# Kernel optimization log

Measured on AMD Instinct MI355X. Metric: run time of the kernel, lower is better.

Reference implementation:

```python
import jax, jax.numpy as jnp
import numpy as np

EMB = 128
BINS = 32
CUT = 5.0
NLAYER = 5
NHID = 4  # extra hidden linears in edge MLP (hidden_dim_list has 5 entries total)
N_NODES = 50000
N_EDGES = 800000
N_GRAPH = 256
NODE_CLASS = 100


def setup_inputs() -> dict:
    key = jax.random.key(0)
    ks = jax.random.split(key, 20)
    s = 0.02
    inp = {
        'z': jax.random.randint(ks[0], (N_NODES,), 0, NODE_CLASS),
        'pos': jax.random.normal(ks[1], (N_NODES, 3), dtype=jnp.float32) * 3.0,
        'batch': jnp.sort(jax.random.randint(ks[2], (N_NODES,), 0, N_GRAPH)),
        'edge_index': jax.random.randint(ks[3], (2, N_EDGES), 0, N_NODES),
        # parameters
        'atom_table': jax.random.normal(ks[4], (NODE_CLASS, EMB), dtype=jnp.float32) * s,
        'atom_w': jax.random.normal(ks[5], (EMB, EMB), dtype=jnp.float32) * s,
        'atom_b': jnp.zeros((EMB,), jnp.float32),
        'edge_emb_w': jax.random.normal(ks[6], (BINS, EMB), dtype=jnp.float32) * s,
        'edge_emb_b': jnp.zeros((EMB,), jnp.float32),
        'edge_w0': jax.random.normal(ks[7], (NLAYER, 3 * EMB, EMB), dtype=jnp.float32) * s,
        'edge_b0': jnp.zeros((NLAYER, EMB), jnp.float32),
        'edge_w': jax.random.normal(ks[8], (NLAYER, NHID, EMB, EMB), dtype=jnp.float32) * s,
        'edge_b': jnp.zeros((NLAYER, NHID, EMB), jnp.float32),
        'node_w': jax.random.normal(ks[9], (NLAYER, EMB, EMB), dtype=jnp.float32) * s,
        'node_b': jnp.zeros((NLAYER, EMB), jnp.float32),
        'out_w': jax.random.normal(ks[10], (EMB, 1), dtype=jnp.float32) * s,
        'out_b': jnp.zeros((1,), jnp.float32),
    }
    return inp


def reference(z, pos, batch, edge_index, atom_table, atom_w, atom_b,
              edge_emb_w, edge_emb_b, edge_w0, edge_b0, edge_w, edge_b,
              node_w, node_b, out_w, out_b):
    silu = jax.nn.silu
    row, col = edge_index[0], edge_index[1]

    # atom embedding + linear
    h_node = atom_table[z] @ atom_w + atom_b  # [N, EMB]

    # edge distances -> gaussian basis expansion (linear spacing, log_base=1.0)
    d = jnp.linalg.norm(pos[row] - pos[col], axis=-1)  # [E]
    mu = jnp.linspace(0.0, CUT, BINS, dtype=jnp.float32)
    sigma = CUT / BINS
    basis = jnp.exp(-0.5 * ((d[:, None] - mu) / sigma) ** 2)  # [E, BINS]
    h_edge = basis @ edge_emb_w + edge_emb_b  # [E, EMB]

    # message passing layers
    for l in range(NLAYER):
        m = jnp.concatenate([h_edge, h_node[row], h_node[col]], axis=-1)  # [E, 3*EMB]
        m = silu(m @ edge_w0[l] + edge_b0[l])
        for k in range(NHID):
            m = silu(m @ edge_w[l, k] + edge_b[l, k])
        h_edge = h_edge + m  # residual edge update
        agg = jax.ops.segment_sum(h_edge, row, num_segments=N_NODES)  # [N, EMB]
        h_node = h_node + silu(agg @ node_w[l] + node_b[l])  # residual node update

    # scatter-mean graph pool
    sums = jax.ops.segment_sum(h_node, batch, num_segments=N_GRAPH)
    cnt = jax.ops.segment_sum(jnp.ones((h_node.shape[0],), h_node.dtype), batch, num_segments=N_GRAPH)
    h_graph = sums / jnp.clip(cnt, 1.0)[:, None]

    return h_graph @ out_w + out_b  # [N_GRAPH, 1]
```

## Files before the change

### kernel.cpp

```cpp
#include <hip/hip_runtime.h>

#define EMB      128
#define N_NODES_ 50000
#define N_EDGES_ 800000
#define N_GRAPH_ 256
#define NLAYER_  5

#define WP_ATOM  573440
#define WP_NODE0 589824
#define WP_EMB   671744
#define WP_TOTAL 675840

typedef short short8 __attribute__((ext_vector_type(8)));
typedef float floatx4 __attribute__((ext_vector_type(4)));

__device__ __forceinline__ float silu_f(float x) {
    return __fdividef(x, 1.0f + __expf(-x));
}
__device__ __forceinline__ float bf2f(unsigned short h) {
    return __uint_as_float(((unsigned)h) << 16);
}
__device__ __forceinline__ unsigned short f2bf(float f) {
    unsigned u = __float_as_uint(f);
    unsigned r = 0x7FFFu + ((u >> 16) & 1u);
    return (unsigned short)((u + r) >> 16);
}

#if defined(__has_builtin)
#if __has_builtin(__builtin_amdgcn_cvt_pk_bf16_f32)
#define HAVE_PK_BF16 1
#endif
#endif
#ifdef HAVE_PK_BF16
typedef __bf16 bf16x2 __attribute__((ext_vector_type(2)));
__device__ __forceinline__ unsigned f2bf_pk(float a, float b) {
    bf16x2 v = __builtin_amdgcn_cvt_pk_bf16_f32(a, b);
    unsigned u;
    __builtin_memcpy(&u, &v, 4);
    return u;
}
#else
__device__ __forceinline__ unsigned f2bf_pk(float a, float b) {
    return (unsigned)f2bf(a) | ((unsigned)f2bf(b) << 16);
}
#endif

__device__ __forceinline__ void wave_lds_fence() {
    __builtin_amdgcn_fence(__ATOMIC_ACQ_REL, "wavefront");
    __builtin_amdgcn_wave_barrier();
}

__device__ __forceinline__ void gload_lds16(const unsigned short* g, unsigned short* l) {
    __builtin_amdgcn_global_load_lds(
        (const __attribute__((address_space(1))) void*)g,
        (__attribute__((address_space(3))) void*)l,
        16, 0, 0);
}

__global__ __launch_bounds__(256) void hist_kernel(
    const int* __restrict__ row, int* __restrict__ hist)
{
    const int e = blockIdx.x * 256 + threadIdx.x;
    if (e < N_EDGES_) atomicAdd(&hist[row[e]], 1);
}

__global__ __launch_bounds__(256) void scan_kernel(
    const int* __restrict__ hist, int* __restrict__ cursor)
{
    __shared__ int ssum[256];
    const int tid = threadIdx.x;
    const int chunk = (N_NODES_ + 255) / 256;
    const int base = tid * chunk;
    int s = 0;
    for (int i = 0; i < chunk; ++i) {
        const int idx = base + i;
        if (idx < N_NODES_) s += hist[idx];
    }
    ssum[tid] = s;
    __syncthreads();
    for (int off = 1; off < 256; off <<= 1) {
        const int t2 = (tid >= off) ? ssum[tid - off] : 0;
        __syncthreads();
        ssum[tid] += t2;
        __syncthreads();
    }
    int run = ssum[tid] - s;
    for (int i = 0; i < chunk; ++i) {
        const int idx = base + i;
        if (idx < N_NODES_) { cursor[idx] = run; run += hist[idx]; }
    }
}

__global__ __launch_bounds__(256) void scatter_kernel(
    const int* __restrict__ row, const int* __restrict__ col,
    int* __restrict__ cursor, int* __restrict__ row_s, int* __restrict__ col_s)
{
    const int e = blockIdx.x * 256 + threadIdx.x;
    if (e >= N_EDGES_) return;
    const int r = row[e];
    const int p = atomicAdd(&cursor[r], 1);
    row_s[p] = r;
    col_s[p] = col[e];
}

__global__ __launch_bounds__(256) void pack_w_kernel(
    const float* __restrict__ edge_w0, const float* __restrict__ edge_w,
    const float* __restrict__ atom_w, const float* __restrict__ node_w,
    const float* __restrict__ edge_emb_w,
    unsigned short* __restrict__ Wp)
{
    const int bid = blockIdx.x;
    int Kb, t;
    const float* src;
    unsigned short* dst;
    if (bid < 200) {
        const int l = bid / 40, r = bid % 40, s = r / 8;
        t = r % 8;
        Kb = (s == 0) ? 12 : 4;
        src = (s == 0) ? edge_w0 + (size_t)l * 384 * 128
                       : edge_w + ((size_t)l * 4 + (s - 1)) * 128 * 128;
        dst = Wp + (size_t)l * 114688 + ((s == 0) ? 0 : (49152 + (s - 1) * 16384))
            + (size_t)t * Kb * 512;
    } else if (bid < 208) {
        t = bid - 200; Kb = 4; src = atom_w;
        dst = Wp + WP_ATOM + (size_t)t * Kb * 512;
    } else if (bid < 248) {
        const int l = (bid - 208) >> 3; t = (bid - 208) & 7; Kb = 4;
        src = node_w + (size_t)l * 128 * 128;
        dst = Wp + WP_NODE0 + (size_t)l * 16384 + (size_t)t * Kb * 512;
    } else {
        t = bid - 248; Kb = 1; src = edge_emb_w;
        dst = Wp + WP_EMB + (size_t)t * 512;
    }
    const int n = Kb * 512;
    for (int p = threadIdx.x; p < n; p += 256) {
        const int j = p & 7, lane = (p >> 3) & 63, kb = p >> 9;
        const int k  = kb * 32 + ((lane >> 4) << 3) + j;
        const int nn = t * 16 + (lane & 15);
        dst[p] = f2bf(src[(size_t)k * 128 + nn]);
    }
}

__global__ __launch_bounds__(256, 5) void edge_mlp_csr_kernel(
    const unsigned short* __restrict__ h_node_bf, unsigned short* __restrict__ h_edge,
    const int* __restrict__ row_s, const int* __restrict__ col_s,
    const unsigned short* __restrict__ Wp,
    const float* __restrict__ b0, const float* __restrict__ bh)
{
    __shared__ __align__(16) unsigned short Xs[8192];
    __shared__ __align__(16) unsigned short Ys[8192];

    const int tid  = threadIdx.x;
    const int e0   = blockIdx.x * 64;
    const int lane = tid & 63;
    const int wv   = tid >> 6;
    const int lr   = lane & 15;
    const int lg   = lane >> 4;
    const int nt0  = 2 * wv, nt1 = nt0 + 1;

    const int t_ = tid >> 2, q_ = tid & 3;
    short8 he_reg[4];
#pragma unroll
    for (int i = 0; i < 4; ++i)
        he_reg[i] = *(const short8*)&h_edge[(size_t)(e0 + t_) * 128 + (q_ + 4 * i) * 8];

    const int srow = 16 * wv + lg;
#pragma unroll
    for (int j = 0; j < 4; ++j) {
        const int r = srow + 4 * j;
        const int c = lr ^ (r & 7);
        gload_lds16(h_edge + (size_t)(e0 + r) * 128 + c * 8,
                    &Xs[(16 * wv + 4 * j) * 128]);
    }
    int cnode[4];
#pragma unroll
    for (int j = 0; j < 4; ++j) {
        const int r = srow + 4 * j;
        const int c = lr ^ (r & 7);
        const int nd = row_s[e0 + r];
        cnode[j] = col_s[e0 + r];
        gload_lds16(h_node_bf + (size_t)nd * 128 + c * 8,
                    &Ys[(16 * wv + 4 * j) * 128]);
    }

    floatx4 acc0[4], acc1[4];
    {
        const float4 bv0 = *(const float4*)&b0[nt0 * 16 + lg * 4];
        const float4 bv1 = *(const float4*)&b0[nt1 * 16 + lg * 4];
#pragma unroll
        for (int et = 0; et < 4; ++et) {
            acc0[et] = (floatx4){bv0.x, bv0.y, bv0.z, bv0.w};
            acc1[et] = (floatx4){bv1.x, bv1.y, bv1.z, bv1.w};
        }
    }
    const unsigned short* aptr0 = Wp + ((size_t)(nt0 * 12) * 64 + lane) * 8;
    const unsigned short* aptr1 = Wp + ((size_t)(nt1 * 12) * 64 + lane) * 8;

    asm volatile("s_waitcnt vmcnt(4)" ::: "memory");
    __syncthreads();

#pragma unroll 2
    for (int kk = 0; kk < 4; ++kk) {
        const short8 wf0 = *(const short8*)(aptr0 + (size_t)kk * 512);
        const short8 wf1 = *(const short8*)(aptr1 + (size_t)kk * 512);
#pragma unroll
        for (int et = 0; et < 4; ++et) {
            const int r = et * 16 + lr;
            const short8 mf = *(const short8*)&Xs[r * 128 + (((kk * 4 + lg) ^ (r & 7)) << 3)];
            acc0[et] = __builtin_amdgcn_mfma_f32_16x16x32_bf16(wf0, mf, acc0[et], 0, 0, 0);
            acc1[et] = __builtin_amdgcn_mfma_f32_16x16x32_bf16(wf1, mf, acc1[et], 0, 0, 0);
        }
    }
    asm volatile("s_waitcnt vmcnt(0)" ::: "memory");
    __syncthreads();

#pragma unroll
    for (int j = 0; j < 4; ++j) {
        const int r = srow + 4 * j;
        const int c = lr ^ (r & 7);
        gload_lds16(h_node_bf + (size_t)cnode[j] * 128 + c * 8,
                    &Xs[(16 * wv + 4 * j) * 128]);
    }

#pragma unroll 2
    for (int kk = 0; kk < 4; ++kk) {
        const short8 wf0 = *(const short8*)(aptr0 + (size_t)(kk + 4) * 512);
        const short8 wf1 = *(const short8*)(aptr1 + (size_t)(kk + 4) * 512);
#pragma unroll
        for (int et = 0; et < 4; ++et) {
            const int r = et * 16 + lr;
            const short8 mf = *(const short8*)&Ys[r * 128 + (((kk * 4 + lg) ^ (r & 7)) << 3)];
            acc0[et] = __builtin_amdgcn_mfma_f32_16x16x32_bf16(wf0, mf, acc0[et], 0, 0, 0);
            acc1[et] = __builtin_amdgcn_mfma_f32_16x16x32_bf16(wf1, mf, acc1[et], 0, 0, 0);
        }
    }
    asm volatile("s_waitcnt vmcnt(0)" ::: "memory");
    __syncthreads();

#pragma unroll 2
    for (int kk = 0; kk < 4; ++kk) {
        const short8 wf0 = *(const short8*)(aptr0 + (size_t)(kk + 8) * 512);
        const short8 wf1 = *(const short8*)(aptr1 + (size_t)(kk + 8) * 512);
#pragma unroll
        for (int et = 0; et < 4; ++et) {
            const int r = et * 16 + lr;
            const short8 mf = *(const short8*)&Xs[r * 128 + (((kk * 4 + lg) ^ (r & 7)) << 3)];
            acc0[et] = __builtin_amdgcn_mfma_f32_16x16x32_bf16(wf0, mf, acc0[et], 0, 0, 0);
            acc1[et] = __builtin_amdgcn_mfma_f32_16x16x32_bf16(wf1, mf, acc1[et], 0, 0, 0);
        }
    }
#pragma unroll
    for (int et = 0; et < 4; ++et) {
        const int r = et * 16 + lr;
        uint2 p0, p1;
        p0.x = f2bf_pk(silu_f(acc0[et][0]), silu_f(acc0[et][1]));
        p0.y = f2bf_pk(silu_f(acc0[et][2]), silu_f(acc0[et][3]));
        p1.x = f2bf_pk(silu_f(acc1[et][0]), silu_f(acc1[et][1]));
        p1.y = f2bf_pk(silu_f(acc1[et][2]), silu_f(acc1[et][3]));
        const int c0 = (2 * nt0 + (lg >> 1)) ^ (r & 7);
        const int c1 = (2 * nt1 + (lg >> 1)) ^ (r & 7);
        *(uint2*)&Ys[r * 128 + c0 * 8 + (lg & 1) * 4] = p0;
        *(uint2*)&Ys[r * 128 + c1 * 8 + (lg & 1) * 4] = p1;
    }
    __syncthreads();

#pragma unroll 1
    for (int s = 1; s < 5; ++s) {
        const unsigned short* bin = (s & 1) ? Ys : Xs;
        unsigned short* bout      = (s & 1) ? Xs : Ys;
        const unsigned short* __restrict__ Ws = Wp + 49152 + (size_t)(s - 1) * 16384;
        const float* __restrict__ bias = bh + (size_t)(s - 1) * 128;

        const float4 bv0 = *(const float4*)&bias[nt0 * 16 + lg * 4];
        const float4 bv1 = *(const float4*)&bias[nt1 * 16 + lg * 4];
#pragma unroll
        for (int et = 0; et < 4; ++et) {
            acc0[et] = (floatx4){bv0.x, bv0.y, bv0.z, bv0.w};
            acc1[et] = (floatx4){bv1.x, bv1.y, bv1.z, bv1.w};
        }
        const unsigned short* ap0 = Ws + ((size_t)(nt0 * 4) * 64 + lane) * 8;
        const unsigned short* ap1 = Ws + ((size_t)(nt1 * 4) * 64 + lane) * 8;
#pragma unroll 2
        for (int kk = 0; kk < 4; ++kk) {
            const short8 wf0 = *(const short8*)(ap0 + (size_t)kk * 512);
            const short8 wf1 = *(const short8*)(ap1 + (size_t)kk * 512);
#pragma unroll
            for (int et = 0; et < 4; ++et) {
                const int r = et * 16 + lr;
                const short8 mf = *(const short8*)&bin[r * 128 + (((kk * 4 + lg) ^ (r & 7)) << 3)];
                acc0[et] = __builtin_amdgcn_mfma_f32_16x16x32_bf16(wf0, mf, acc0[et], 0, 0, 0);
                acc1[et] = __builtin_amdgcn_mfma_f32_16x16x32_bf16(wf1, mf, acc1[et], 0, 0, 0);
            }
        }
#pragma unroll
        for (int et = 0; et < 4; ++et) {
            const int r = et * 16 + lr;
            uint2 p0, p1;
            p0.x = f2bf_pk(silu_f(acc0[et][0]), silu_f(acc0[et][1]));
            p0.y = f2bf_pk(silu_f(acc0[et][2]), silu_f(acc0[et][3]));
            p1.x = f2bf_pk(silu_f(acc1[et][0]), silu_f(acc1[et][1]));
            p1.y = f2bf_pk(silu_f(acc1[et][2]), silu_f(acc1[et][3]));
            const int c0 = (2 * nt0 + (lg >> 1)) ^ (r & 7);
            const int c1 = (2 * nt1 + (lg >> 1)) ^ (r & 7);
            *(uint2*)&bout[r * 128 + c0 * 8 + (lg & 1) * 4] = p0;
            *(uint2*)&bout[r * 128 + c1 * 8 + (lg & 1) * 4] = p1;
        }
        __syncthreads();
    }

#pragma unroll
    for (int i = 0; i < 4; ++i) {
        const int ch = q_ + 4 * i;
        const short8 mv = *(const short8*)&Ys[t_ * 128 + ((ch ^ (t_ & 7)) << 3)];
        const short8 ov = he_reg[i];
        float he[8];
#pragma unroll
        for (int j = 0; j < 8; ++j)
            he[j] = bf2f((unsigned short)ov[j]) + bf2f((unsigned short)mv[j]);
        uint4 sv;
        sv.x = f2bf_pk(he[0], he[1]);
        sv.y = f2bf_pk(he[2], he[3]);
        sv.z = f2bf_pk(he[4], he[5]);
        sv.w = f2bf_pk(he[6], he[7]);
        *(uint4*)(h_edge + (size_t)(e0 + t_) * 128 + ch * 8) = sv;
    }
}

__global__ __launch_bounds__(256, 4) void node_agg_gemm_kernel(
    const unsigned short* __restrict__ h_edge,
    const int* __restrict__ hist, const int* __restrict__ cur_end,
    const unsigned short* __restrict__ Wpm, const float* __restrict__ bias,
    unsigned short* __restrict__ h_node_bf, int N)
{
    __shared__ __align__(16) unsigned short B[64][136];
    const int tid  = threadIdx.x;
    const int lane = tid & 63;
    const int wv   = tid >> 6;
    const int n0   = blockIdx.x * 64;

    {
        const int t = tid >> 2, q = tid & 3;
        const int n = n0 + t;
        float a[32];
#pragma unroll
        for (int j = 0; j < 32; ++j) a[j] = 0.f;
        if (n < N) {
            const int e_end = cur_end[n];
            const int e_beg = e_end - hist[n];
            for (int e = e_beg; e < e_end; ++e) {
                const unsigned short* p = &h_edge[(size_t)e * 128 + q * 32];
#pragma unroll
                for (int g = 0; g < 4; ++g) {
                    const short8 v = *(const short8*)(p + g * 8);
#pragma unroll
                    for (int j = 0; j < 8; ++j)
                        a[g * 8 + j] += bf2f((unsigned short)v[j]);
                }
            }
        }
#pragma unroll
        for (int g = 0; g < 4; ++g) {
            uint4 pk;
            pk.x = f2bf_pk(a[g * 8 + 0], a[g * 8 + 1]);
            pk.y = f2bf_pk(a[g * 8 + 2], a[g * 8 + 3]);
            pk.z = f2bf_pk(a[g * 8 + 4], a[g * 8 + 5]);
            pk.w = f2bf_pk(a[g * 8 + 6], a[g * 8 + 7]);
            *(uint4*)&B[t][q * 32 + g * 8] = pk;
        }
    }
    wave_lds_fence();

    const int lr = lane & 15, lg = lane >> 4;
    floatx4 acc[8];
#pragma unroll
    for (int nt = 0; nt < 8; ++nt) {
        const float4 bv = *(const float4*)&bias[nt * 16 + lg * 4];
        acc[nt] = (floatx4){bv.x, bv.y, bv.z, bv.w};
    }
    const unsigned short* brow = &B[wv * 16 + lr][0];
#pragma unroll 2
    for (int kb = 0; kb < 4; ++kb) {
        const short8 mf = *(const short8*)(brow + kb * 32 + lg * 8);
#pragma unroll
        for (int nt = 0; nt < 8; ++nt) {
            const short8 wf = *(const short8*)(Wpm + ((size_t)(nt * 4 + kb) * 64 + lane) * 8);
            acc[nt] = __builtin_amdgcn_mfma_f32_16x16x32_bf16(wf, mf, acc[nt], 0, 0, 0);
        }
    }
    const int node = n0 + wv * 16 + lr;
    if (node < N) {
        unsigned short* drow = &h_node_bf[(size_t)node * 128];
#pragma unroll
        for (int nt = 0; nt < 8; ++nt) {
            float x0 = silu_f(acc[nt][0]), x1 = silu_f(acc[nt][1]);
            float x2 = silu_f(acc[nt][2]), x3 = silu_f(acc[nt][3]);
            unsigned short* p = drow + nt * 16 + lg * 4;
            const uint2 d = *(const uint2*)p;
            x0 += bf2f((unsigned short)(d.x & 0xFFFF));
            x1 += bf2f((unsigned short)(d.x >> 16));
            x2 += bf2f((unsigned short)(d.y & 0xFFFF));
            x3 += bf2f((unsigned short)(d.y >> 16));
            uint2 o;
            o.x = f2bf_pk(x0, x1);
            o.y = f2bf_pk(x2, x3);
            *(uint2*)p = o;
        }
    }
}

__global__ __launch_bounds__(256, 4) void atom_gemm_mfma_kernel(
    const float* __restrict__ src, const int* __restrict__ gidx,
    const unsigned short* __restrict__ Wpm, const float* __restrict__ bias,
    unsigned short* __restrict__ dst, int N)
{
    __shared__ __align__(16) unsigned short B[64][136];
    const int tid  = threadIdx.x;
    const int lane = tid & 63;
    const int wv   = tid >> 6;
    const int n0   = blockIdx.x * 64;

    {
        const int t = tid >> 2, q = tid & 3;
        const int node = n0 + t;
        const float* srow = src;
        if (node < N) srow = &src[(size_t)gidx[node] * 128];
#pragma unroll
        for (int i = 0; i < 4; ++i) {
            const int k8 = (q + 4 * i) << 3;
            uint4 pk = make_uint4(0, 0, 0, 0);
            if (node < N) {
                const float4 f0 = *(const float4*)(srow + k8);
                const float4 f1 = *(const float4*)(srow + k8 + 4);
                pk.x = f2bf_pk(f0.x, f0.y);
                pk.y = f2bf_pk(f0.z, f0.w);
                pk.z = f2bf_pk(f1.x, f1.y);
                pk.w = f2bf_pk(f1.z, f1.w);
            }
            *(uint4*)&B[t][k8] = pk;
        }
    }
    wave_lds_fence();

    const int lr = lane & 15, lg = lane >> 4;
    floatx4 acc[8];
#pragma unroll
    for (int nt = 0; nt < 8; ++nt) {
        const float4 bv = *(const float4*)&bias[nt * 16 + lg * 4];
        acc[nt] = (floatx4){bv.x, bv.y, bv.z, bv.w};
    }
    const unsigned short* brow = &B[wv * 16 + lr][0];
#pragma unroll 2
    for (int kb = 0; kb < 4; ++kb) {
        const short8 mf = *(const short8*)(brow + kb * 32 + lg * 8);
#pragma unroll
        for (int nt = 0; nt < 8; ++nt) {
            const short8 wf = *(const short8*)(Wpm + ((size_t)(nt * 4 + kb) * 64 + lane) * 8);
            acc[nt] = __builtin_amdgcn_mfma_f32_16x16x32_bf16(wf, mf, acc[nt], 0, 0, 0);
        }
    }
    const int node = n0 + wv * 16 + lr;
    if (node < N) {
        unsigned short* drow = &dst[(size_t)node * 128];
#pragma unroll
        for (int nt = 0; nt < 8; ++nt) {
            uint2 o;
            o.x = f2bf_pk(acc[nt][0], acc[nt][1]);
            o.y = f2bf_pk(acc[nt][2], acc[nt][3]);
            *(uint2*)(drow + nt * 16 + lg * 4) = o;
        }
    }
}

__global__ __launch_bounds__(256, 4) void edge_embed_mfma_kernel(
    const float* __restrict__ pos, const int* __restrict__ row, const int* __restrict__ col,
    const unsigned short* __restrict__ Wpe, const float* __restrict__ bemb,
    unsigned short* __restrict__ h_edge)
{
    __shared__ __align__(16) unsigned short Bas[64][40];
    const int tid  = threadIdx.x;
    const int lane = tid & 63;
    const int wv   = tid >> 6;
    const int e0   = blockIdx.x * 64;

    {
        const int t = tid >> 2, q = tid & 3;
        const int rr = row[e0 + t], cc = col[e0 + t];
        const float dx = pos[rr * 3 + 0] - pos[cc * 3 + 0];
        const float dy = pos[rr * 3 + 1] - pos[cc * 3 + 1];
        const float dz = pos[rr * 3 + 2] - pos[cc * 3 + 2];
        const float d = sqrtf(dx * dx + dy * dy + dz * dz);
        const float invs = 32.0f / 5.0f;
        float e[8];
#pragma unroll
        for (int j = 0; j < 8; ++j) {
            const float mu = (float)(q * 8 + j) * (5.0f / 31.0f);
            const float tt = (d - mu) * invs;
            e[j] = __expf(-0.5f * tt * tt);
        }
        uint4 pk;
        pk.x = f2bf_pk(e[0], e[1]);
        pk.y = f2bf_pk(e[2], e[3]);
        pk.z = f2bf_pk(e[4], e[5]);
        pk.w = f2bf_pk(e[6], e[7]);
        *(uint4*)&Bas[t][q * 8] = pk;
    }
    wave_lds_fence();

    const int lr = lane & 15, lg = lane >> 4;
    floatx4 acc[8];
#pragma unroll
    for (int nt = 0; nt < 8; ++nt) {
        const float4 bv = *(const float4*)&bemb[nt * 16 + lg * 4];
        acc[nt] = (floatx4){bv.x, bv.y, bv.z, bv.w};
    }
    const short8 mf = *(const short8*)&Bas[wv * 16 + lr][lg * 8];
#pragma unroll
    for (int nt = 0; nt < 8; ++nt) {
        const short8 wf = *(const short8*)(Wpe + ((size_t)nt * 64 + lane) * 8);
        acc[nt] = __builtin_amdgcn_mfma_f32_16x16x32_bf16(wf, mf, acc[nt], 0, 0, 0);
    }
    unsigned short* erow = &h_edge[(size_t)(e0 + wv * 16 + lr) * 128];
#pragma unroll
    for (int nt = 0; nt < 8; ++nt) {
        uint2 o;
        o.x = f2bf_pk(acc[nt][0], acc[nt][1]);
        o.y = f2bf_pk(acc[nt][2], acc[nt][3]);
        *(uint2*)(erow + nt * 16 + lg * 4) = o;
    }
}

__global__ __launch_bounds__(128) void pool_kernel(
    const unsigned short* __restrict__ h_node_bf, const int* __restrict__ batch,
    float* __restrict__ sums, float* __restrict__ cnt, int N)
{
    __shared__ int bb[256];
    const int tid = threadIdx.x;
    const int n0 = blockIdx.x * 256;
    for (int idx = tid; idx < 256; idx += 128) {
        int n = n0 + idx;
        bb[idx] = (n < N) ? batch[n] : -1;
    }
    __syncthreads();
    int cur = bb[0];
    float run = 0.f, runc = 0.f;
    for (int i = 0; i < 256; ++i) {
        const int b = bb[i];
        if (b < 0) break;
        if (b != cur) {
            atomicAdd(&sums[(size_t)cur * 128 + tid], run);
            if (tid == 0) atomicAdd(&cnt[cur], runc);
            run = 0.f; runc = 0.f; cur = b;
        }
        run += bf2f(h_node_bf[(size_t)(n0 + i) * 128 + tid]);
        runc += 1.f;
    }
    atomicAdd(&sums[(size_t)cur * 128 + tid], run);
    if (tid == 0) atomicAdd(&cnt[cur], runc);
}

__global__ __launch_bounds__(256) void final_kernel(
    const float* __restrict__ sums, const float* __restrict__ cnt,
    const float* __restrict__ out_w, const float* __restrict__ out_b,
    float* __restrict__ out)
{
    const int g = threadIdx.x;
    const float c = fmaxf(cnt[g], 1.0f);
    float acc = 0.f;
    for (int jj = 0; jj < 128; ++jj) acc = fmaf(sums[(size_t)g * 128 + jj], out_w[jj], acc);
    out[g] = acc / c + out_b[0];
}

__global__ void zero_out_kernel(float* out, int n) {
    int i = blockIdx.x * 256 + threadIdx.x;
    if (i < n) out[i] = 0.f;
}


extern "C" void kernel_launch(void* const* d_in, const int* in_sizes, int n_in,
                              void* d_out, int out_size, void* d_ws, size_t ws_size,
                              hipStream_t stream)
{
    const int*   z          = (const int*)  d_in[0];
    const float* pos        = (const float*)d_in[1];
    const int*   batch      = (const int*)  d_in[2];
    const int*   eidx       = (const int*)  d_in[3];
    const float* atom_table = (const float*)d_in[4];
    const float* atom_w     = (const float*)d_in[5];
    const float* atom_b     = (const float*)d_in[6];
    const float* edge_emb_w = (const float*)d_in[7];
    const float* edge_emb_b = (const float*)d_in[8];
    const float* edge_w0    = (const float*)d_in[9];
    const float* edge_b0    = (const float*)d_in[10];
    const float* edge_w     = (const float*)d_in[11];
    const float* edge_b     = (const float*)d_in[12];
    const float* node_w     = (const float*)d_in[13];
    const float* node_b     = (const float*)d_in[14];
    const float* out_w      = (const float*)d_in[15];
    const float* out_b      = (const float*)d_in[16];
    const int* row = eidx;
    const int* col = eidx + N_EDGES_;

    float* aggb = (float*)d_ws;
    float* sums = aggb + (size_t)N_NODES_ * EMB;
    float* cnt  = sums + (size_t)N_GRAPH_ * EMB;
    unsigned short* h_node_bf = (unsigned short*)(cnt + N_GRAPH_);
    unsigned short* h_edge    = h_node_bf + (size_t)N_NODES_ * EMB;
    unsigned short* Wp        = h_edge + (size_t)N_EDGES_ * EMB;
    int* hist   = (int*)(Wp + WP_TOTAL);
    int* cursor = hist + N_NODES_;
    int* row_s  = cursor + N_NODES_;
    int* col_s  = row_s + N_EDGES_;

    const size_t need = ((size_t)(N_NODES_ * EMB + N_GRAPH_ * EMB + N_GRAPH_)) * 4
                      + ((size_t)N_NODES_ * EMB + (size_t)N_EDGES_ * EMB + (size_t)WP_TOTAL) * 2
                      + ((size_t)N_NODES_ * 2 + (size_t)N_EDGES_ * 2) * 4;

    if (ws_size < need) {
        zero_out_kernel<<<1, 256, 0, stream>>>((float*)d_out, N_GRAPH_);
        return;
    }

    const int grid_rows64 = (N_NODES_ + 63) / 64;

    (void)hipMemsetAsync(hist, 0, N_NODES_ * sizeof(int), stream);
    hist_kernel<<<(N_EDGES_ + 255) / 256, 256, 0, stream>>>(row, hist);
    scan_kernel<<<1, 256, 0, stream>>>(hist, cursor);
    scatter_kernel<<<(N_EDGES_ + 255) / 256, 256, 0, stream>>>(row, col, cursor, row_s, col_s);

    pack_w_kernel<<<256, 256, 0, stream>>>(edge_w0, edge_w, atom_w, node_w, edge_emb_w, Wp);

    atom_gemm_mfma_kernel<<<grid_rows64, 256, 0, stream>>>(
        atom_table, z, Wp + WP_ATOM, atom_b, h_node_bf, N_NODES_);
    edge_embed_mfma_kernel<<<N_EDGES_ / 64, 256, 0, stream>>>(
        pos, row_s, col_s, Wp + WP_EMB, edge_emb_b, h_edge);

    for (int l = 0; l < NLAYER_; ++l) {
        edge_mlp_csr_kernel<<<N_EDGES_ / 64, 256, 0, stream>>>(
            h_node_bf, h_edge, row_s, col_s,
            Wp + (size_t)l * 114688,
            edge_b0 + (size_t)l * 128, edge_b + (size_t)l * 4 * 128);
        node_agg_gemm_kernel<<<grid_rows64, 256, 0, stream>>>(
            h_edge, hist, cursor,
            Wp + WP_NODE0 + (size_t)l * 16384, node_b + (size_t)l * 128,
            h_node_bf, N_NODES_);
    }

    (void)hipMemsetAsync(sums, 0, ((size_t)N_GRAPH_ * EMB + N_GRAPH_) * sizeof(float), stream);
    pool_kernel<<<(N_NODES_ + 255) / 256, 128, 0, stream>>>(h_node_bf, batch, sums, cnt, N_NODES_);
    final_kernel<<<1, 256, 0, stream>>>(sums, cnt, out_w, out_b, (float*)d_out);
}
```

Before: 2.556 ms.

## Precompute per-node projections of first edge-MLP layer and gather them per edge

The first edge linear over [h_edge, h_node[row], h_node[col]] is split algebraically. The node parts (W_row·h_node and W_col·h_node) are computed once per node in a new GEMM kernel and stored in bf16 buffers that reuse the aggregation workspace. Each edge then only gathers these projected vectors into its accumulators and runs the h_edge part of the GEMM. This removes two thirds of the first-layer MFMA work over 800k edges and the LDS staging of gathered node rows, at the cost of an extra kernel per layer and an extra bf16 rounding of the projected node terms.

```diff
diff --git a/kernel.cpp b/kernel.cpp
--- a/kernel.cpp
+++ b/kernel.cpp
@@ -141,11 +141,72 @@
     }
 }
 
+__global__ __launch_bounds__(256, 4) void u_gemm_kernel(
+    const unsigned short* __restrict__ h_node_bf,
+    const unsigned short* __restrict__ Wp0, const float* __restrict__ b0,
+    unsigned short* __restrict__ Ur, unsigned short* __restrict__ Uc, int N)
+{
+    __shared__ __align__(16) unsigned short B[64][136];
+    const int tid  = threadIdx.x;
+    const int lane = tid & 63;
+    const int wv   = tid >> 6;
+    const int n0   = blockIdx.x * 64;
+
+    {
+        const int t = tid >> 2, q = tid & 3;
+        const int node = n0 + t;
+#pragma unroll
+        for (int i = 0; i < 4; ++i) {
+            const int k8 = (q + 4 * i) << 3;
+            short8 v = (short8){0,0,0,0,0,0,0,0};
+            if (node < N) v = *(const short8*)&h_node_bf[(size_t)node * 128 + k8];
+            *(short8*)&B[t][k8] = v;
+        }
+    }
+    wave_lds_fence();
+
+    const int lr = lane & 15, lg = lane >> 4;
+    floatx4 accr[8], accc[8];
+#pragma unroll
+    for (int nt = 0; nt < 8; ++nt) {
+        const float4 bv = *(const float4*)&b0[nt * 16 + lg * 4];
+        accr[nt] = (floatx4){bv.x, bv.y, bv.z, bv.w};
+        accc[nt] = (floatx4){0.f, 0.f, 0.f, 0.f};
+    }
+    const unsigned short* brow = &B[wv * 16 + lr][0];
+#pragma unroll 2
+    for (int kb = 0; kb < 4; ++kb) {
+        const short8 mf = *(const short8*)(brow + kb * 32 + lg * 8);
+#pragma unroll
+        for (int nt = 0; nt < 8; ++nt) {
+            const short8 wr = *(const short8*)(Wp0 + ((size_t)(nt * 12 + 4 + kb) * 64 + lane) * 8);
+            const short8 wc = *(const short8*)(Wp0 + ((size_t)(nt * 12 + 8 + kb) * 64 + lane) * 8);
+            accr[nt] = __builtin_amdgcn_mfma_f32_16x16x32_bf16(wr, mf, accr[nt], 0, 0, 0);
+            accc[nt] = __builtin_amdgcn_mfma_f32_16x16x32_bf16(wc, mf, accc[nt], 0, 0, 0);
+        }
+    }
+    const int node = n0 + wv * 16 + lr;
+    if (node < N) {
+        unsigned short* rrow = Ur + (size_t)node * 128;
+        unsigned short* crow = Uc + (size_t)node * 128;
+#pragma unroll
+        for (int nt = 0; nt < 8; ++nt) {
+            uint2 o;
+            o.x = f2bf_pk(accr[nt][0], accr[nt][1]);
+            o.y = f2bf_pk(accr[nt][2], accr[nt][3]);
+            *(uint2*)(rrow + nt * 16 + lg * 4) = o;
+            o.x = f2bf_pk(accc[nt][0], accc[nt][1]);
+            o.y = f2bf_pk(accc[nt][2], accc[nt][3]);
+            *(uint2*)(crow + nt * 16 + lg * 4) = o;
+        }
+    }
+}
+
 __global__ __launch_bounds__(256, 5) void edge_mlp_csr_kernel(
-    const unsigned short* __restrict__ h_node_bf, unsigned short* __restrict__ h_edge,
+    const unsigned short* __restrict__ h_edge,
+    const unsigned short* __restrict__ Ur, const unsigned short* __restrict__ Uc,
     const int* __restrict__ row_s, const int* __restrict__ col_s,
-    const unsigned short* __restrict__ Wp,
-    const float* __restrict__ b0, const float* __restrict__ bh)
+    const unsigned short* __restrict__ Wp, const float* __restrict__ bh)
 {
     __shared__ __align__(16) unsigned short Xs[8192];
     __shared__ __align__(16) unsigned short Ys[8192];
@@ -158,11 +219,13 @@
     const int lg   = lane >> 4;
     const int nt0  = 2 * wv, nt1 = nt0 + 1;
 
-    const int t_ = tid >> 2, q_ = tid & 3;
-    short8 he_reg[4];
-#pragma unroll
-    for (int i = 0; i < 4; ++i)
-        he_reg[i] = *(const short8*)&h_edge[(size_t)(e0 + t_) * 128 + (q_ + 4 * i) * 8];
+    int rid[4], cid[4];
+#pragma unroll
+    for (int et = 0; et < 4; ++et) {
+        const int e = e0 + et * 16 + lr;
+        rid[et] = row_s[e];
+        cid[et] = col_s[e];
+    }
 
     const int srow = 16 * wv + lg;
 #pragma unroll
@@ -172,33 +235,34 @@
         gload_lds16(h_edge + (size_t)(e0 + r) * 128 + c * 8,
                     &Xs[(16 * wv + 4 * j) * 128]);
     }
-    int cnode[4];
-#pragma unroll
-    for (int j = 0; j < 4; ++j) {
-        const int r = srow + 4 * j;
-        const int c = lr ^ (r & 7);
-        const int nd = row_s[e0 + r];
-        cnode[j] = col_s[e0 + r];
-        gload_lds16(h_node_bf + (size_t)nd * 128 + c * 8,
-                    &Ys[(16 * wv + 4 * j) * 128]);
-    }
+
+    uint2 gr0[4], gr1[4], gc0[4], gc1[4];
+#pragma unroll
+    for (int et = 0; et < 4; ++et) {
+        gr0[et] = *(const uint2*)(Ur + (size_t)rid[et] * 128 + nt0 * 16 + lg * 4);
+        gr1[et] = *(const uint2*)(Ur + (size_t)rid[et] * 128 + nt1 * 16 + lg * 4);
+        gc0[et] = *(const uint2*)(Uc + (size_t)cid[et] * 128 + nt0 * 16 + lg * 4);
+        gc1[et] = *(const uint2*)(Uc + (size_t)cid[et] * 128 + nt1 * 16 + lg * 4);
+    }
+
+    asm volatile("s_waitcnt vmcnt(0)" ::: "memory");
+    __syncthreads();
 
     floatx4 acc0[4], acc1[4];
-    {
-        const float4 bv0 = *(const float4*)&b0[nt0 * 16 + lg * 4];
-        const float4 bv1 = *(const float4*)&b0[nt1 * 16 + lg * 4];
-#pragma unroll
-        for (int et = 0; et < 4; ++et) {
-            acc0[et] = (floatx4){bv0.x, bv0.y, bv0.z, bv0.w};
-            acc1[et] = (floatx4){bv1.x, bv1.y, bv1.z, bv1.w};
-        }
-    }
+#pragma unroll
+    for (int et = 0; et < 4; ++et) {
+        acc0[et][0] = bf2f((unsigned short)(gr0[et].x & 0xFFFF)) + bf2f((unsigned short)(gc0[et].x & 0xFFFF));
+        acc0[et][1] = bf2f((unsigned short)(gr0[et].x >> 16))    + bf2f((unsigned short)(gc0[et].x >> 16));
+        acc0[et][2] = bf2f((unsigned short)(gr0[et].y & 0xFFFF)) + bf2f((unsigned short)(gc0[et].y & 0xFFFF));
+        acc0[et][3] = bf2f((unsigned short)(gr0[et].y >> 16))    + bf2f((unsigned short)(gc0[et].y >> 16));
+        acc1[et][0] = bf2f((unsigned short)(gr1[et].x & 0xFFFF)) + bf2f((unsigned short)(gc1[et].x & 0xFFFF));
+        acc1[et][1] = bf2f((unsigned short)(gr1[et].x >> 16))    + bf2f((unsigned short)(gc1[et].x >> 16));
+        acc1[et][2] = bf2f((unsigned short)(gr1[et].y & 0xFFFF)) + bf2f((unsigned short)(gc1[et].y & 0xFFFF));
+        acc1[et][3] = bf2f((unsigned short)(gr1[et].y >> 16))    + bf2f((unsigned short)(gc1[et].y >> 16));
+    }
+
     const unsigned short* aptr0 = Wp + ((size_t)(nt0 * 12) * 64 + lane) * 8;
     const unsigned short* aptr1 = Wp + ((size_t)(nt1 * 12) * 64 + lane) * 8;
-
-    asm volatile("s_waitcnt vmcnt(4)" ::: "memory");
-    __syncthreads();
-
 #pragma unroll 2
     for (int kk = 0; kk < 4; ++kk) {
         const short8 wf0 = *(const short8*)(aptr0 + (size_t)kk * 512);
@@ -211,44 +275,15 @@
             acc1[et] = __builtin_amdgcn_mfma_f32_16x16x32_bf16(wf1, mf, acc1[et], 0, 0, 0);
         }
     }
-    asm volatile("s_waitcnt vmcnt(0)" ::: "memory");
-    __syncthreads();
-
-#pragma unroll
-    for (int j = 0; j < 4; ++j) {
-        const int r = srow + 4 * j;
-        const int c = lr ^ (r & 7);
-        gload_lds16(h_node_bf + (size_t)cnode[j] * 128 + c * 8,
-                    &Xs[(16 * wv + 4 * j) * 128]);
-    }
-
-#pragma unroll 2
-    for (int kk = 0; kk < 4; ++kk) {
-        const short8 wf0 = *(const short8*)(aptr0 + (size_t)(kk + 4) * 512);
-        const short8 wf1 = *(const short8*)(aptr1 + (size_t)(kk + 4) * 512);
-#pragma unroll
-        for (int et = 0; et < 4; ++et) {
-            const int r = et * 16 + lr;
-            const short8 mf = *(const short8*)&Ys[r * 128 + (((kk * 4 + lg) ^ (r & 7)) << 3)];
-            acc0[et] = __builtin_amdgcn_mfma_f32_16x16x32_bf16(wf0, mf, acc0[et], 0, 0, 0);
-            acc1[et] = __builtin_amdgcn_mfma_f32_16x16x32_bf16(wf1, mf, acc1[et], 0, 0, 0);
-        }
-    }
-    asm volatile("s_waitcnt vmcnt(0)" ::: "memory");
-    __syncthreads();
-
-#pragma unroll 2
-    for (int kk = 0; kk < 4; ++kk) {
-        const short8 wf0 = *(const short8*)(aptr0 + (size_t)(kk + 8) * 512);
-        const short8 wf1 = *(const short8*)(aptr1 + (size_t)(kk + 8) * 512);
-#pragma unroll
-        for (int et = 0; et < 4; ++et) {
-            const int r = et * 16 + lr;
-            const short8 mf = *(const short8*)&Xs[r * 128 + (((kk * 4 + lg) ^ (r & 7)) << 3)];
-            acc0[et] = __builtin_amdgcn_mfma_f32_16x16x32_bf16(wf0, mf, acc0[et], 0, 0, 0);
-            acc1[et] = __builtin_amdgcn_mfma_f32_16x16x32_bf16(wf1, mf, acc1[et], 0, 0, 0);
-        }
-    }
+
+    const int t_ = tid >> 2, q_ = tid & 3;
+    short8 he_reg[4];
+#pragma unroll
+    for (int i = 0; i < 4; ++i) {
+        const int ch = q_ + 4 * i;
+        he_reg[i] = *(const short8*)&Xs[t_ * 128 + ((ch ^ (t_ & 7)) << 3)];
+    }
+
 #pragma unroll
     for (int et = 0; et < 4; ++et) {
         const int r = et * 16 + lr;
@@ -322,7 +357,7 @@
         sv.y = f2bf_pk(he[2], he[3]);
         sv.z = f2bf_pk(he[4], he[5]);
         sv.w = f2bf_pk(he[6], he[7]);
-        *(uint4*)(h_edge + (size_t)(e0 + t_) * 128 + ch * 8) = sv;
+        *(uint4*)(const_cast<unsigned short*>(h_edge) + (size_t)(e0 + t_) * 128 + ch * 8) = sv;
     }
 }
 
@@ -611,6 +646,9 @@
     int* row_s  = cursor + N_NODES_;
     int* col_s  = row_s + N_EDGES_;
 
+    unsigned short* Ur = (unsigned short*)aggb;
+    unsigned short* Uc = Ur + (size_t)N_NODES_ * EMB;
+
     const size_t need = ((size_t)(N_NODES_ * EMB + N_GRAPH_ * EMB + N_GRAPH_)) * 4
                       + ((size_t)N_NODES_ * EMB + (size_t)N_EDGES_ * EMB + (size_t)WP_TOTAL) * 2
                       + ((size_t)N_NODES_ * 2 + (size_t)N_EDGES_ * 2) * 4;
@@ -635,10 +673,13 @@
         pos, row_s, col_s, Wp + WP_EMB, edge_emb_b, h_edge);
 
     for (int l = 0; l < NLAYER_; ++l) {
+        u_gemm_kernel<<<grid_rows64, 256, 0, stream>>>(
+            h_node_bf, Wp + (size_t)l * 114688, edge_b0 + (size_t)l * 128,
+            Ur, Uc, N_NODES_);
         edge_mlp_csr_kernel<<<N_EDGES_ / 64, 256, 0, stream>>>(
-            h_node_bf, h_edge, row_s, col_s,
+            h_edge, Ur, Uc, row_s, col_s,
             Wp + (size_t)l * 114688,
-            edge_b0 + (size_t)l * 128, edge_b + (size_t)l * 4 * 128);
+            edge_b + (size_t)l * 4 * 128);
         node_agg_gemm_kernel<<<grid_rows64, 256, 0, stream>>>(
             h_edge, hist, cursor,
             Wp + WP_NODE0 + (size_t)l * 16384, node_b + (size_t)l * 128,
```

Result: no change. 2.532 ms (-1.0%).
